# Kernel optimization log

Measured on AMD Instinct MI355X. Metric: run time of the kernel, lower is better.

## Reference

```python
import jax, jax.numpy as jnp
import numpy as np

H, W = 2048, 2048
N = H * W
MEAN_MODULO = 1.0


def setup_inputs() -> dict:
    key = jax.random.key(0)
    k1, k2, k3 = jax.random.split(key, 3)
    pred_E = jax.random.uniform(k1, (N,), dtype=jnp.float32)
    pred_v = jax.random.uniform(k2, (N,), dtype=jnp.float32)
    strain = jax.random.normal(k3, (N, 3), dtype=jnp.float32)
    return {"pred_E": pred_E, "pred_v": pred_v, "strain": strain}


def _conv_valid(x_hw, k_33):
    # x_hw: [H, W] -> NHWC [1,H,W,1]; k_33: [3,3] -> HWIO [3,3,1,1]; cross-correlation, VALID
    x = x_hw[None, :, :, None]
    k = k_33[:, :, None, None]
    y = jax.lax.conv_general_dilated(
        x, k, window_strides=(1, 1), padding="VALID",
        dimension_numbers=("NHWC", "HWIO", "NHWC"))
    return y[0, :, :, 0]  # [H-2, W-2]


def reference(pred_E, pred_v, strain):
    # ---- calculate_stress (closed-form batched plane-stress constitutive law) ----
    v = pred_v
    e0, e1, e2 = strain[:, 0], strain[:, 1], strain[:, 2]
    # strain[i] @ [[1,v,0],[v,1,0],[0,0,(1-v)/2]]
    s0 = e0 + v * e1
    s1 = v * e0 + e1
    s2 = e2 * (1.0 - v) * 0.5
    frac = pred_E / (1.0 - v * v)          # E / (1 - v^2), broadcast over 3 components
    stress = jnp.stack([s0, s1, s2], axis=1) * frac[:, None]  # [N, 3]

    # ---- calculate_loss_r (FD equilibrium residuals via 3x3 stencils) ----
    sum_k = jnp.ones((3, 3), dtype=jnp.float32)
    wx_xx = jnp.array([[-1., -1., -1.], [0., 0., 0.], [1., 1., 1.]], dtype=jnp.float32)
    wx_xy = jnp.array([[1., 0., -1.], [1., 0., -1.], [1., 0., -1.]], dtype=jnp.float32)
    wy_yy = wx_xy
    wy_xy = wx_xx

    E_mat = pred_E.reshape(H, W)
    sxx = stress[:, 0].reshape(H, W)
    syy = stress[:, 1].reshape(H, W)
    sxy = stress[:, 2].reshape(H, W)

    E_conv = _conv_valid(E_mat, sum_k)
    fx = _conv_valid(sxx, wx_xx) + _conv_valid(sxy, wx_xy)
    fy = _conv_valid(syy, wy_yy) + _conv_valid(sxy, wy_xy)

    loss_x = jnp.mean(jnp.abs(fx / E_conv))
    loss_y = jnp.mean(jnp.abs(fy / E_conv))
    loss_e = jnp.abs(jnp.mean(pred_E) - MEAN_MODULO)
    return loss_x + loss_y + loss_e / 100.0
```

## Files before the change

kernel.cpp:

```cpp
#include <hip/hip_runtime.h>
#include <math.h>

#define HH 2048
#define WW 2048
#define TILE 32
#define ROWS 34
#define QC   9
#define LSTRIDE 36
#define NBLK (64 * 64)

__device__ __forceinline__ float rcpf(float x) { return __builtin_amdgcn_rcpf(x); }

__global__ __launch_bounds__(256) void fused_loss_kernel(
    const float* __restrict__ pred_E,
    const float* __restrict__ pred_v,
    const float* __restrict__ strain,
    float* __restrict__ part)
{
    __shared__ float sE [ROWS][LSTRIDE];
    __shared__ float sxx[ROWS][LSTRIDE];
    __shared__ float syy[ROWS][LSTRIDE];
    __shared__ float sxy[ROWS][LSTRIDE];

    const int tid = threadIdx.x;
    const int r0 = blockIdx.y * TILE, c0 = blockIdx.x * TILE;

    float4 E4[2], V4[2], SA[2], SB[2], SC[2];
    int rr[2], qq[2];
    bool ld[2];
    #pragma unroll
    for (int it = 0; it < 2; ++it) {
        const int idx = tid + it * 256;
        const int r = idx / QC;
        const int q = idx - r * QC;
        rr[it] = r; qq[it] = q;
        const int gi = r0 + r;
        const int gc = c0 + q * 4;
        const bool a = (idx < ROWS * QC) && (gi < HH) && (gc < WW);
        ld[it] = a;
        if (a) {
            const int g = gi * WW + gc;
            E4[it] = *(const float4*)(pred_E + g);
            V4[it] = *(const float4*)(pred_v + g);
            const float* sp = strain + 3 * g;
            SA[it] = *(const float4*)(sp);
            SB[it] = *(const float4*)(sp + 4);
            SC[it] = *(const float4*)(sp + 8);
        }
    }

    float sumE = 0.f;
    #pragma unroll
    for (int it = 0; it < 2; ++it) {
        if (ld[it]) {
            const int r = rr[it], q = qq[it];
            const float e[4]  = {E4[it].x, E4[it].y, E4[it].z, E4[it].w};
            const float vv[4] = {V4[it].x, V4[it].y, V4[it].z, V4[it].w};
            const float s0[4] = {SA[it].x, SA[it].w, SB[it].z, SC[it].y};
            const float s1[4] = {SA[it].y, SB[it].x, SB[it].w, SC[it].z};
            const float s2[4] = {SA[it].z, SB[it].y, SC[it].x, SC[it].w};
            float xx[4], yy[4], xy[4];
            #pragma unroll
            for (int p = 0; p < 4; ++p) {
                const float v  = vv[p];
                const float fr = e[p] * rcpf(1.f - v * v);
                xx[p] = (s0[p] + v * s1[p]) * fr;
                yy[p] = (v * s0[p] + s1[p]) * fr;
                xy[p] = (s2[p] * (1.f - v) * 0.5f) * fr;
            }
            const int cq = 4 * q;
            *(float4*)&sE [r][cq] = E4[it];
            *(float4*)&sxx[r][cq] = make_float4(xx[0], xx[1], xx[2], xx[3]);
            *(float4*)&syy[r][cq] = make_float4(yy[0], yy[1], yy[2], yy[3]);
            *(float4*)&sxy[r][cq] = make_float4(xy[0], xy[1], xy[2], xy[3]);
            if (r < TILE && q < 8)
                sumE += e[0] + e[1] + e[2] + e[3];
        }
    }
    __syncthreads();

    const int tx = tid & 31;
    const int ty = tid >> 5;
    const int lb = ty * 4;

    float rsE[6], rsxx[6], rsxy[6], xyL[6], xyR[6], yyL[6], yyR[6];
    #pragma unroll
    for (int i = 0; i < 6; ++i) {
        const int r = lb + i;
        rsE[i]  = sE [r][tx] + sE [r][tx + 1] + sE [r][tx + 2];
        rsxx[i] = sxx[r][tx] + sxx[r][tx + 1] + sxx[r][tx + 2];
        const float l = sxy[r][tx], m = sxy[r][tx + 1], rg = sxy[r][tx + 2];
        xyL[i] = l; xyR[i] = rg; rsxy[i] = l + m + rg;
        yyL[i] = syy[r][tx]; yyR[i] = syy[r][tx + 2];
    }

    float ax = 0.f, ay = 0.f;
    const bool cok = (c0 + tx) < (WW - 2);
    #pragma unroll
    for (int k = 0; k < 4; ++k) {
        const int gi = r0 + lb + k;
        if (cok && gi < (HH - 2)) {
            const float rEc = rcpf(rsE[k] + rsE[k + 1] + rsE[k + 2]);
            const float fx = (rsxx[k + 2] - rsxx[k])
                           + (xyL[k] + xyL[k + 1] + xyL[k + 2])
                           - (xyR[k] + xyR[k + 1] + xyR[k + 2]);
            const float fy = (yyL[k] + yyL[k + 1] + yyL[k + 2])
                           - (yyR[k] + yyR[k + 1] + yyR[k + 2])
                           + (rsxy[k + 2] - rsxy[k]);
            ax += fabsf(fx) * rEc;
            ay += fabsf(fy) * rEc;
        }
    }

    #pragma unroll
    for (int off = 32; off > 0; off >>= 1) {
        ax   += __shfl_down(ax, off);
        ay   += __shfl_down(ay, off);
        sumE += __shfl_down(sumE, off);
    }
    __shared__ float red[3][4];
    const int wave = tid >> 6, lane = tid & 63;
    if (lane == 0) { red[0][wave] = ax; red[1][wave] = ay; red[2][wave] = sumE; }
    __syncthreads();
    if (tid == 0) {
        const int b = blockIdx.y * 64 + blockIdx.x;
        part[b]            = red[0][0] + red[0][1] + red[0][2] + red[0][3];
        part[NBLK + b]     = red[1][0] + red[1][1] + red[1][2] + red[1][3];
        part[2 * NBLK + b] = red[2][0] + red[2][1] + red[2][2] + red[2][3];
    }
}

__global__ __launch_bounds__(256) void finalize_kernel(
    const float* __restrict__ part, float* __restrict__ out)
{
    const int tid = threadIdx.x;
    const float4* px = (const float4*)(part);
    const float4* py = (const float4*)(part + NBLK);
    const float4* pe = (const float4*)(part + 2 * NBLK);
    float x = 0.f, y = 0.f, e = 0.f;
    #pragma unroll
    for (int k = 0; k < 4; ++k) {
        const int i = tid + k * 256;
        const float4 a = px[i], b = py[i], c = pe[i];
        x += a.x + a.y + a.z + a.w;
        y += b.x + b.y + b.z + b.w;
        e += c.x + c.y + c.z + c.w;
    }
    #pragma unroll
    for (int off = 32; off > 0; off >>= 1) {
        x += __shfl_down(x, off);
        y += __shfl_down(y, off);
        e += __shfl_down(e, off);
    }
    __shared__ float red[3][4];
    const int wave = tid >> 6, lane = tid & 63;
    if (lane == 0) { red[0][wave] = x; red[1][wave] = y; red[2][wave] = e; }
    __syncthreads();
    if (tid == 0) {
        const float rx = red[0][0] + red[0][1] + red[0][2] + red[0][3];
        const float ry = red[1][0] + red[1][1] + red[1][2] + red[1][3];
        const float re = red[2][0] + red[2][1] + red[2][2] + red[2][3];
        const float M = (float)((HH - 2) * (WW - 2));
        const float loss_x = rx / M;
        const float loss_y = ry / M;
        const float loss_e = fabsf(re / (float)(HH * WW) - 1.0f);
        out[0] = loss_x + loss_y + loss_e * 0.01f;
    }
}

extern "C" void kernel_launch(void* const* d_in, const int* in_sizes, int n_in,
                              void* d_out, int out_size, void* d_ws, size_t ws_size,
                              hipStream_t stream) {
    const float* pred_E = (const float*)d_in[0];
    const float* pred_v = (const float*)d_in[1];
    const float* strain = (const float*)d_in[2];
    float* out  = (float*)d_out;
    float* part = (float*)d_ws;

    dim3 grid(WW / TILE, HH / TILE);
    fused_loss_kernel<<<grid, 256, 0, stream>>>(pred_E, pred_v, strain, part);
    finalize_kernel<<<1, 256, 0, stream>>>(part, out);
}
```

Before: 110.4 us.

## Process two tiles per block, prefetching second tile during first stencil

Each block now handles two adjacent 32x32 tiles. The global loads for the second tile are issued into registers before the stencil on the first tile runs, so load latency overlaps with compute. The grid is halved, and the partial-sum count and finalize loop are adjusted to match. A launch-bounds occupancy hint is added. The costs are higher register pressure from holding two stages of loads and an extra barrier per block.

```diff
diff --git a/kernel.cpp b/kernel.cpp
--- a/kernel.cpp
+++ b/kernel.cpp
@@ -7,58 +7,56 @@
 #define ROWS 34
 #define QC   9
 #define LSTRIDE 36
-#define NBLK (64 * 64)
+#define NBLK (32 * 64)
 
 __device__ __forceinline__ float rcpf(float x) { return __builtin_amdgcn_rcpf(x); }
 
-__global__ __launch_bounds__(256) void fused_loss_kernel(
-    const float* __restrict__ pred_E,
-    const float* __restrict__ pred_v,
-    const float* __restrict__ strain,
-    float* __restrict__ part)
-{
-    __shared__ float sE [ROWS][LSTRIDE];
-    __shared__ float sxx[ROWS][LSTRIDE];
-    __shared__ float syy[ROWS][LSTRIDE];
-    __shared__ float sxy[ROWS][LSTRIDE];
-
-    const int tid = threadIdx.x;
-    const int r0 = blockIdx.y * TILE, c0 = blockIdx.x * TILE;
-
-    float4 E4[2], V4[2], SA[2], SB[2], SC[2];
-    int rr[2], qq[2];
-    bool ld[2];
+struct StageRegs {
+    float4 E, V, A, B, C;
+    int r, q;
+    bool ld;
+};
+
+__device__ __forceinline__ void stage_load(
+    const float* __restrict__ pred_E, const float* __restrict__ pred_v,
+    const float* __restrict__ strain, int r0, int c0, int tid, StageRegs R[2])
+{
     #pragma unroll
     for (int it = 0; it < 2; ++it) {
         const int idx = tid + it * 256;
         const int r = idx / QC;
         const int q = idx - r * QC;
-        rr[it] = r; qq[it] = q;
+        R[it].r = r; R[it].q = q;
         const int gi = r0 + r;
         const int gc = c0 + q * 4;
         const bool a = (idx < ROWS * QC) && (gi < HH) && (gc < WW);
-        ld[it] = a;
+        R[it].ld = a;
         if (a) {
             const int g = gi * WW + gc;
-            E4[it] = *(const float4*)(pred_E + g);
-            V4[it] = *(const float4*)(pred_v + g);
+            R[it].E = *(const float4*)(pred_E + g);
+            R[it].V = *(const float4*)(pred_v + g);
             const float* sp = strain + 3 * g;
-            SA[it] = *(const float4*)(sp);
-            SB[it] = *(const float4*)(sp + 4);
-            SC[it] = *(const float4*)(sp + 8);
+            R[it].A = *(const float4*)(sp);
+            R[it].B = *(const float4*)(sp + 4);
+            R[it].C = *(const float4*)(sp + 8);
         }
     }
-
-    float sumE = 0.f;
+}
+
+__device__ __forceinline__ void stage_math_store(
+    StageRegs R[2], float& sumE,
+    float (*sE)[LSTRIDE], float (*sxx)[LSTRIDE],
+    float (*syy)[LSTRIDE], float (*sxy)[LSTRIDE])
+{
     #pragma unroll
     for (int it = 0; it < 2; ++it) {
-        if (ld[it]) {
-            const int r = rr[it], q = qq[it];
-            const float e[4]  = {E4[it].x, E4[it].y, E4[it].z, E4[it].w};
-            const float vv[4] = {V4[it].x, V4[it].y, V4[it].z, V4[it].w};
-            const float s0[4] = {SA[it].x, SA[it].w, SB[it].z, SC[it].y};
-            const float s1[4] = {SA[it].y, SB[it].x, SB[it].w, SC[it].z};
-            const float s2[4] = {SA[it].z, SB[it].y, SC[it].x, SC[it].w};
+        if (R[it].ld) {
+            const int r = R[it].r, q = R[it].q;
+            const float e[4]  = {R[it].E.x, R[it].E.y, R[it].E.z, R[it].E.w};
+            const float vv[4] = {R[it].V.x, R[it].V.y, R[it].V.z, R[it].V.w};
+            const float s0[4] = {R[it].A.x, R[it].A.w, R[it].B.z, R[it].C.y};
+            const float s1[4] = {R[it].A.y, R[it].B.x, R[it].B.w, R[it].C.z};
+            const float s2[4] = {R[it].A.z, R[it].B.y, R[it].C.x, R[it].C.w};
             float xx[4], yy[4], xy[4];
             #pragma unroll
             for (int p = 0; p < 4; ++p) {
@@ -69,7 +67,7 @@
                 xy[p] = (s2[p] * (1.f - v) * 0.5f) * fr;
             }
             const int cq = 4 * q;
-            *(float4*)&sE [r][cq] = E4[it];
+            *(float4*)&sE [r][cq] = R[it].E;
             *(float4*)&sxx[r][cq] = make_float4(xx[0], xx[1], xx[2], xx[3]);
             *(float4*)&syy[r][cq] = make_float4(yy[0], yy[1], yy[2], yy[3]);
             *(float4*)&sxy[r][cq] = make_float4(xy[0], xy[1], xy[2], xy[3]);
@@ -77,8 +75,13 @@
                 sumE += e[0] + e[1] + e[2] + e[3];
         }
     }
-    __syncthreads();
-
+}
+
+__device__ __forceinline__ void stencil(
+    int r0, int c0, int tid, float& ax, float& ay,
+    float (*sE)[LSTRIDE], float (*sxx)[LSTRIDE],
+    float (*syy)[LSTRIDE], float (*sxy)[LSTRIDE])
+{
     const int tx = tid & 31;
     const int ty = tid >> 5;
     const int lb = ty * 4;
@@ -94,7 +97,6 @@
         yyL[i] = syy[r][tx]; yyR[i] = syy[r][tx + 2];
     }
 
-    float ax = 0.f, ay = 0.f;
     const bool cok = (c0 + tx) < (WW - 2);
     #pragma unroll
     for (int k = 0; k < 4; ++k) {
@@ -111,6 +113,35 @@
             ay += fabsf(fy) * rEc;
         }
     }
+}
+
+__global__ __launch_bounds__(256, 4) void fused_loss_kernel(
+    const float* __restrict__ pred_E,
+    const float* __restrict__ pred_v,
+    const float* __restrict__ strain,
+    float* __restrict__ part)
+{
+    __shared__ float sE [ROWS][LSTRIDE];
+    __shared__ float sxx[ROWS][LSTRIDE];
+    __shared__ float syy[ROWS][LSTRIDE];
+    __shared__ float sxy[ROWS][LSTRIDE];
+
+    const int tid = threadIdx.x;
+    const int r0 = blockIdx.y * TILE;
+    const int c0 = blockIdx.x * (2 * TILE);
+
+    float sumE = 0.f, ax = 0.f, ay = 0.f;
+    StageRegs R0[2], R1[2];
+
+    stage_load(pred_E, pred_v, strain, r0, c0, tid, R0);
+    stage_math_store(R0, sumE, sE, sxx, syy, sxy);
+    __syncthreads();
+    stage_load(pred_E, pred_v, strain, r0, c0 + TILE, tid, R1);
+    stencil(r0, c0, tid, ax, ay, sE, sxx, syy, sxy);
+    __syncthreads();
+    stage_math_store(R1, sumE, sE, sxx, syy, sxy);
+    __syncthreads();
+    stencil(r0, c0 + TILE, tid, ax, ay, sE, sxx, syy, sxy);
 
     #pragma unroll
     for (int off = 32; off > 0; off >>= 1) {
@@ -123,7 +154,7 @@
     if (lane == 0) { red[0][wave] = ax; red[1][wave] = ay; red[2][wave] = sumE; }
     __syncthreads();
     if (tid == 0) {
-        const int b = blockIdx.y * 64 + blockIdx.x;
+        const int b = blockIdx.y * 32 + blockIdx.x;
         part[b]            = red[0][0] + red[0][1] + red[0][2] + red[0][3];
         part[NBLK + b]     = red[1][0] + red[1][1] + red[1][2] + red[1][3];
         part[2 * NBLK + b] = red[2][0] + red[2][1] + red[2][2] + red[2][3];
@@ -139,7 +170,7 @@
     const float4* pe = (const float4*)(part + 2 * NBLK);
     float x = 0.f, y = 0.f, e = 0.f;
     #pragma unroll
-    for (int k = 0; k < 4; ++k) {
+    for (int k = 0; k < 2; ++k) {
         const int i = tid + k * 256;
         const float4 a = px[i], b = py[i], c = pe[i];
         x += a.x + a.y + a.z + a.w;
@@ -177,7 +208,7 @@
     float* out  = (float*)d_out;
     float* part = (float*)d_ws;
 
-    dim3 grid(WW / TILE, HH / TILE);
+    dim3 grid(WW / (2 * TILE), HH / TILE);
     fused_loss_kernel<<<grid, 256, 0, stream>>>(pred_E, pred_v, strain, part);
     finalize_kernel<<<1, 256, 0, stream>>>(part, out);
 }
```

Result: no change. 109.9 us, median of 2 (-0.4%).
